# Optimization experiments

Hardware: AMD Instinct MI355X
Metric: run time of the kernel (lower is better)

The kernel has to match this reference:

```python
import jax, jax.numpy as jnp
import numpy as np

B, N, D, H = 2, 2048, 1024, 16
HD = D // H

def setup_inputs() -> dict:
    key = jax.random.key(0)
    ks = jax.random.split(key, 8)
    s = lambda fan_in: 1.0 / np.sqrt(fan_in)
    return {
        "x": jax.random.normal(ks[0], (B, N, D), jnp.float32),
        "coverage": jax.random.uniform(ks[1], (B, N, 1), jnp.float32),
        "w_qkv": jax.random.normal(ks[2], (D, 3 * D), jnp.float32) * s(D),
        "w_out": jax.random.normal(ks[3], (D, D), jnp.float32) * s(D),
        "b_out": jnp.zeros((D,), jnp.float32),
        "w_ce1": jax.random.normal(ks[4], (1, D // 4), jnp.float32),
        "b_ce1": jnp.zeros((D // 4,), jnp.float32),
        "w_ce2": jax.random.normal(ks[5], (D // 4, H), jnp.float32) * s(D // 4),
        "b_ce2": jnp.zeros((H,), jnp.float32),
        "w_fg1": jax.random.normal(ks[6], (D, D // 4), jnp.float32) * s(D),
        "b_fg1": jnp.zeros((D // 4,), jnp.float32),
        "w_fg2": jax.random.normal(ks[7], (D // 4, 1), jnp.float32) * s(D // 4),
        "b_fg2": jnp.zeros((1,), jnp.float32),
    }

def reference(x, coverage, w_qkv, w_out, b_out, w_ce1, b_ce1, w_ce2, b_ce2,
              w_fg1, b_fg1, w_fg2, b_fg2):
    b, n, d = x.shape
    h = w_ce2.shape[1]
    hd = d // h
    scale = hd ** -0.5
    qkv = x @ w_qkv  # (B,N,3D)
    q, k, v = jnp.split(qkv, 3, axis=-1)
    q = q.reshape(b, n, h, hd).transpose(0, 2, 1, 3)  # (B,H,N,hd)
    k = k.reshape(b, n, h, hd).transpose(0, 2, 1, 3)
    v = v.reshape(b, n, h, hd).transpose(0, 2, 1, 3)
    attn = jnp.einsum("bhnd,bhmd->bhnm", q, k) * scale  # (B,H,N,N)
    # coverage bias: MLP(1 -> D/4 -> H), broadcast over query dim
    cov = jax.nn.silu(coverage @ w_ce1 + b_ce1) @ w_ce2 + b_ce2  # (B,N,H)
    cov_bias = cov.transpose(0, 2, 1)[:, :, None, :]  # (B,H,1,N)
    # fusion gate on mean-pooled features
    x_pooled = x.mean(axis=1)  # (B,D)
    g = jax.nn.sigmoid(jax.nn.silu(x_pooled @ w_fg1 + b_fg1) @ w_fg2 + b_fg2)  # (B,1)
    g = g[:, :, None, None]  # (B,1,1,1)
    # g*(attn+bias) + (1-g)*attn == attn + g*bias (exact same math)
    attn = attn + g * cov_bias
    attn = jax.nn.softmax(attn, axis=-1)
    out = jnp.einsum("bhnm,bhmd->bhnd", attn, v)  # (B,H,N,hd)
    out = out.transpose(0, 2, 1, 3).reshape(b, n, d)
    return out @ w_out + b_out
```

## Files before the change

### kernel.cpp

```cpp
#include <hip/hip_runtime.h>
#include <math.h>

typedef __bf16 bf16_t;
typedef __bf16 bf16x8 __attribute__((ext_vector_type(8)));
typedef __bf16 bf16x4 __attribute__((ext_vector_type(4)));
typedef float f32x4 __attribute__((ext_vector_type(4)));

#define MFMA16(a, b, c) __builtin_amdgcn_mfma_f32_16x16x32_bf16((a), (b), (c), 0, 0, 0)

constexpr int Bc = 2, Nc = 2048, Dc = 1024, Hc = 16, HDc = 64;
constexpr float C1 = 0.18033688011112042f;
constexpr float LOG2E = 1.4426950408889634f;

__device__ __forceinline__ void glds16(const bf16_t* g, bf16_t* l) {
    __builtin_amdgcn_global_load_lds(
        (const __attribute__((address_space(1))) unsigned int*)g,
        (__attribute__((address_space(3))) unsigned int*)l, 16, 0, 0);
}

__global__ __launch_bounds__(256) void prep_all(const float* __restrict__ x,
                                                const float* __restrict__ w_qkv,
                                                const float* __restrict__ w_out,
                                                const float* __restrict__ coverage,
                                                const float* __restrict__ w_ce1,
                                                const float* __restrict__ b_ce1,
                                                const float* __restrict__ w_ce2,
                                                const float* __restrict__ b_ce2,
                                                bf16_t* __restrict__ Xb,
                                                bf16_t* __restrict__ Wt,
                                                bf16_t* __restrict__ WoT,
                                                float* __restrict__ pooled,
                                                float* __restrict__ biasbuf) {
    __shared__ bf16_t tile[64 * 66];
    int blk = blockIdx.x, t = threadIdx.x;
    if (blk < 512) {
        int row0 = blk * 8;
        int b = row0 >> 11;
        int c = t * 4;
        float s0 = 0.f, s1 = 0.f, s2 = 0.f, s3 = 0.f;
#pragma unroll
        for (int rr = 0; rr < 8; ++rr) {
            size_t off = (size_t)(row0 + rr) * 1024 + c;
            float4 v = *(const float4*)(x + off);
            bf16x4 o = { (bf16_t)v.x, (bf16_t)v.y, (bf16_t)v.z, (bf16_t)v.w };
            *(bf16x4*)(Xb + off) = o;
            s0 += v.x; s1 += v.y; s2 += v.z; s3 += v.w;
        }
        atomicAdd(&pooled[b * 1024 + c + 0], s0);
        atomicAdd(&pooled[b * 1024 + c + 1], s1);
        atomicAdd(&pooled[b * 1024 + c + 2], s2);
        atomicAdd(&pooled[b * 1024 + c + 3], s3);
    } else if (blk < 1536) {
        int idx = blk - 512;
        int cx = idx & 63, ry = idx >> 6;
        const float* src; bf16_t* dst; int C;
        if (cx < 48) { src = w_qkv; dst = Wt; C = 3072; }
        else         { src = w_out; dst = WoT; C = 1024; cx -= 48; }
        const int R = 1024;
        int r0 = ry * 64, c0 = cx * 64;
        int cl = t & 63, rl = t >> 6;
#pragma unroll
        for (int p = 0; p < 16; ++p) {
            int r = p * 4 + rl;
            tile[r * 66 + cl] = (bf16_t)src[(size_t)(r0 + r) * C + c0 + cl];
        }
        __syncthreads();
#pragma unroll
        for (int p = 0; p < 16; ++p) {
            int r = p * 4 + rl;
            dst[(size_t)(c0 + r) * R + r0 + cl] = tile[cl * 66 + r];
        }
    } else {
        int cb = blk - 1536;
        int h = t & 15;
        int gn = cb * 16 + (t >> 4);
        int b = gn >> 11, n = gn & 2047;
        float c = coverage[gn];
        float acc = b_ce2[h];
        for (int j = 0; j < 256; ++j) {
            float tv = c * w_ce1[j] + b_ce1[j];
            tv = tv / (1.0f + __expf(-tv));
            acc += tv * w_ce2[j * 16 + h];
        }
        biasbuf[((size_t)b * 16 + h) * 2048 + n] = LOG2E * acc;
    }
}

__global__ __launch_bounds__(256) void gate1(const float* __restrict__ pooled,
                                             const float* __restrict__ w_fg1,
                                             const float* __restrict__ b_fg1,
                                             const float* __restrict__ w_fg2,
                                             float* __restrict__ hacc) {
    int b = blockIdx.x >> 8, j = blockIdx.x & 255;
    int t = threadIdx.x;
    float p = 0.f;
#pragma unroll
    for (int i = 0; i < 4; ++i) {
        int d = t * 4 + i;
        p += pooled[b * 1024 + d] * w_fg1[d * 256 + j];
    }
#pragma unroll
    for (int off = 32; off > 0; off >>= 1) p += __shfl_down(p, off);
    __shared__ float red[4];
    if ((t & 63) == 0) red[t >> 6] = p;
    __syncthreads();
    if (t == 0) {
        float hj = (red[0] + red[1] + red[2] + red[3]) * (1.0f / 2048.0f) + b_fg1[j];
        hj = hj / (1.0f + __expf(-hj));
        atomicAdd(&hacc[b], hj * w_fg2[j]);
    }
}

__global__ __launch_bounds__(256) void gatebias(float* __restrict__ biasbuf,
                                                const float* __restrict__ hacc,
                                                const float* __restrict__ b_fg2) {
    int idx = (blockIdx.x * 256 + threadIdx.x) * 4;
    int b = idx >> 15;
    float g = 1.0f / (1.0f + __expf(-(hacc[b] + b_fg2[0])));
    float4 v = *(const float4*)(biasbuf + idx);
    v.x *= g; v.y *= g; v.z *= g; v.w *= g;
    *(float4*)(biasbuf + idx) = v;
}

__global__ __launch_bounds__(256) void qk_gemm(const bf16_t* __restrict__ Xb,
                                               const bf16_t* __restrict__ Wt,
                                               bf16_t* __restrict__ Q,
                                               bf16_t* __restrict__ Kb) {
    __shared__ __align__(16) bf16_t At[128 * 64];
    __shared__ __align__(16) bf16_t Bt[128 * 64];
    int t = threadIdx.x, w = t >> 6, lane = t & 63;
    int l16 = lane & 15, quad = lane >> 4;
    int wm = w & 1, wx = w >> 1;
    int m0 = blockIdx.x * 128;
    int n0 = blockIdx.y * 128;
    f32x4 acc[4][4] = {};
    int swl = l16 & 7;

    for (int k0 = 0; k0 < 1024; k0 += 64) {
#pragma unroll
        for (int i = 0; i < 4; ++i) {
            int fb = i * 4096 + w * 1024;
            int f = fb + lane * 16;
            int row = f >> 7;
            int ch = (f >> 4) & 7;
            int sc = ch ^ (row & 7);
            glds16(Wt + (size_t)(n0 + row) * 1024 + k0 + sc * 8, At + (fb >> 1));
            glds16(Xb + (size_t)(m0 + row) * 1024 + k0 + sc * 8, Bt + (fb >> 1));
        }
        __syncthreads();
#pragma unroll
        for (int s = 0; s < 2; ++s) {
            bf16x8 afr[4], bfr[4];
#pragma unroll
            for (int mi = 0; mi < 4; ++mi)
                afr[mi] = *(const bf16x8*)(At + (wm * 64 + mi * 16 + l16) * 64 + (((s * 4 + quad) ^ swl) * 8));
#pragma unroll
            for (int ni = 0; ni < 4; ++ni)
                bfr[ni] = *(const bf16x8*)(Bt + (wx * 64 + ni * 16 + l16) * 64 + (((s * 4 + quad) ^ swl) * 8));
#pragma unroll
            for (int mi = 0; mi < 4; ++mi)
#pragma unroll
                for (int ni = 0; ni < 4; ++ni)
                    acc[mi][ni] = MFMA16(afr[mi], bfr[ni], acc[mi][ni]);
        }
        __syncthreads();
    }

    int sec = n0 >> 10;
    bf16_t* dst = (sec == 0 ? Q : Kb);
#pragma unroll
    for (int mi = 0; mi < 4; ++mi) {
        int gc = n0 + wm * 64 + mi * 16 + quad * 4;
        int dcol = gc & 1023;
        int h = dcol >> 6, hd = dcol & 63;
#pragma unroll
        for (int ni = 0; ni < 4; ++ni) {
            int gx = m0 + wx * 64 + ni * 16 + l16;
            int b = gx >> 11, n = gx & 2047;
            size_t bh = (size_t)(b * 16 + h);
            bf16x4 pk = { (bf16_t)acc[mi][ni][0], (bf16_t)acc[mi][ni][1],
                          (bf16_t)acc[mi][ni][2], (bf16_t)acc[mi][ni][3] };
            *(bf16x4*)(dst + (bh * 2048 + n) * 64 + hd) = pk;
        }
    }
}

__global__ __launch_bounds__(256) void v_gemm(const bf16_t* __restrict__ Xb,
                                              const bf16_t* __restrict__ Wt,
                                              bf16_t* __restrict__ Vt) {
    __shared__ __align__(16) bf16_t At[128 * 64];
    __shared__ __align__(16) bf16_t Bt[128 * 64];
    int t = threadIdx.x, w = t >> 6, lane = t & 63;
    int l16 = lane & 15, quad = lane >> 4;
    int wm = w & 1, wx = w >> 1;
    int n0 = blockIdx.x * 128;
    int m0 = blockIdx.y * 128;
    const bf16_t* WtV = Wt + (size_t)2048 * 1024;
    f32x4 acc[4][4] = {};
    int swl = l16 & 7;

    for (int k0 = 0; k0 < 1024; k0 += 64) {
#pragma unroll
        for (int i = 0; i < 4; ++i) {
            int fb = i * 4096 + w * 1024;
            int f = fb + lane * 16;
            int row = f >> 7;
            int ch = (f >> 4) & 7;
            int sc = ch ^ (row & 7);
            glds16(Xb + (size_t)(m0 + row) * 1024 + k0 + sc * 8, At + (fb >> 1));
            glds16(WtV + (size_t)(n0 + row) * 1024 + k0 + sc * 8, Bt + (fb >> 1));
        }
        __syncthreads();
#pragma unroll
        for (int s = 0; s < 2; ++s) {
            bf16x8 afr[4], bfr[4];
#pragma unroll
            for (int mi = 0; mi < 4; ++mi)
                afr[mi] = *(const bf16x8*)(At + (wm * 64 + mi * 16 + l16) * 64 + (((s * 4 + quad) ^ swl) * 8));
#pragma unroll
            for (int ni = 0; ni < 4; ++ni)
                bfr[ni] = *(const bf16x8*)(Bt + (wx * 64 + ni * 16 + l16) * 64 + (((s * 4 + quad) ^ swl) * 8));
#pragma unroll
            for (int mi = 0; mi < 4; ++mi)
#pragma unroll
                for (int ni = 0; ni < 4; ++ni)
                    acc[mi][ni] = MFMA16(afr[mi], bfr[ni], acc[mi][ni]);
        }
        __syncthreads();
    }

#pragma unroll
    for (int mi = 0; mi < 4; ++mi) {
        int rowx = m0 + wm * 64 + mi * 16 + quad * 4;
        int b = rowx >> 11, n = rowx & 2047;
        int np = (n & ~31) + ((n >> 2) & 3) * 8 + ((n >> 4) & 1) * 4;
#pragma unroll
        for (int ni = 0; ni < 4; ++ni) {
            int colv = n0 + wx * 64 + ni * 16 + l16;
            int h = colv >> 6, hd = colv & 63;
            bf16x4 pk = { (bf16_t)acc[mi][ni][0], (bf16_t)acc[mi][ni][1],
                          (bf16_t)acc[mi][ni][2], (bf16_t)acc[mi][ni][3] };
            *(bf16x4*)(Vt + ((size_t)(b * 16 + h) * 64 + hd) * 2048 + np) = pk;
        }
    }
}

__global__ __launch_bounds__(256) void attn_k(const bf16_t* __restrict__ Q,
                                              const bf16_t* __restrict__ Kb,
                                              const bf16_t* __restrict__ Vt,
                                              const float* __restrict__ biasbuf,
                                              bf16_t* __restrict__ O) {
    __shared__ __align__(16) bf16_t kbuf[2][64 * 64];
    __shared__ __align__(16) bf16_t vbuf[2][64 * 64];
    int t = threadIdx.x, w = t >> 6, lane = t & 63;
    int l16 = lane & 15, quad = lane >> 4;
    int bh = blockIdx.y;
    int b = bh >> 4, h = bh & 15;
    int qa = blockIdx.x * 128 + w * 32;
    const bf16_t* Qh = Q + (size_t)bh * 2048 * 64;
    const bf16_t* Kh = Kb + (size_t)bh * 2048 * 64;
    const bf16_t* Vh = Vt + (size_t)bh * 64 * 2048;
    const float* bih = biasbuf + (size_t)bh * 2048;

    int fb0 = w * 2048, fb1 = fb0 + 1024;
    int f0 = fb0 + lane * 16, f1 = fb1 + lane * 16;
    int krow0 = f0 >> 7, kch0 = ((f0 >> 4) & 7) ^ (krow0 & 7);
    int krow1 = f1 >> 7, kch1 = ((f1 >> 4) & 7) ^ (krow1 & 7);

    bf16x8 qf[2][2];
#pragma unroll
    for (int g = 0; g < 2; ++g)
#pragma unroll
        for (int dh = 0; dh < 2; ++dh)
            qf[g][dh] = *(const bf16x8*)(Qh + (size_t)(qa + g * 16 + l16) * 64 + dh * 32 + quad * 8);

    f32x4 o[2][4] = {};
    f32x4 osum[2] = {};
    const f32x4 zero = { 0.f, 0.f, 0.f, 0.f };
    int swl = l16 & 7;
    bf16x8 ones;
#pragma unroll
    for (int i = 0; i < 8; ++i) ones[i] = (bf16_t)1.0f;

    {
        glds16(Kh + (size_t)krow0 * 64 + kch0 * 8, &kbuf[0][fb0 >> 1]);
        glds16(Kh + (size_t)krow1 * 64 + kch1 * 8, &kbuf[0][fb1 >> 1]);
        glds16(Vh + (size_t)krow0 * 2048 + kch0 * 8, &vbuf[0][fb0 >> 1]);
        glds16(Vh + (size_t)krow1 * 2048 + kch1 * 8, &vbuf[0][fb1 >> 1]);
    }

    for (int it = 0; it < 32; ++it) {
        int j0 = it * 64, sel = it & 1;
        __syncthreads();
        if (it + 1 < 32) {
            int jn = j0 + 64, sn = sel ^ 1;
            glds16(Kh + (size_t)(jn + krow0) * 64 + kch0 * 8, &kbuf[sn][fb0 >> 1]);
            glds16(Kh + (size_t)(jn + krow1) * 64 + kch1 * 8, &kbuf[sn][fb1 >> 1]);
            glds16(Vh + (size_t)krow0 * 2048 + jn + kch0 * 8, &vbuf[sn][fb0 >> 1]);
            glds16(Vh + (size_t)krow1 * 2048 + jn + kch1 * 8, &vbuf[sn][fb1 >> 1]);
        }
        const bf16_t* kb = kbuf[sel];
        const bf16_t* vb = vbuf[sel];

        float4 bias[4];
#pragma unroll
        for (int kt = 0; kt < 4; ++kt)
            bias[kt] = *(const float4*)(bih + j0 + kt * 16 + quad * 4);

        f32x4 s[4][2];
#pragma unroll
        for (int kt = 0; kt < 4; ++kt) {
            bf16x8 kf0 = *(const bf16x8*)(kb + (kt * 16 + l16) * 64 + ((quad ^ swl) * 8));
            bf16x8 kf1 = *(const bf16x8*)(kb + (kt * 16 + l16) * 64 + (((4 + quad) ^ swl) * 8));
#pragma unroll
            for (int g = 0; g < 2; ++g) {
                s[kt][g] = MFMA16(kf0, qf[g][0], zero);
                s[kt][g] = MFMA16(kf1, qf[g][1], s[kt][g]);
            }
        }

#pragma unroll
        for (int kt = 0; kt < 4; ++kt) {
            const float* bp = (const float*)&bias[kt];
#pragma unroll
            for (int g = 0; g < 2; ++g)
#pragma unroll
                for (int r = 0; r < 4; ++r)
                    s[kt][g][r] = __builtin_amdgcn_exp2f(s[kt][g][r] * C1 + bp[r]);
        }

        bf16x8 pf[2][2];
#pragma unroll
        for (int g = 0; g < 2; ++g)
#pragma unroll
            for (int pv = 0; pv < 2; ++pv) {
                bf16x8 tmp;
#pragma unroll
                for (int i = 0; i < 4; ++i) {
                    tmp[i]     = (bf16_t)s[2 * pv][g][i];
                    tmp[i + 4] = (bf16_t)s[2 * pv + 1][g][i];
                }
                pf[g][pv] = tmp;
            }

#pragma unroll
        for (int dt = 0; dt < 4; ++dt) {
            const bf16_t* vrow = vb + (dt * 16 + l16) * 64;
#pragma unroll
            for (int pv = 0; pv < 2; ++pv) {
                bf16x8 vf = *(const bf16x8*)(vrow + (((pv * 4 + quad) ^ swl) * 8));
#pragma unroll
                for (int g = 0; g < 2; ++g)
                    o[g][dt] = MFMA16(pf[g][pv], vf, o[g][dt]);
            }
        }
#pragma unroll
        for (int g = 0; g < 2; ++g) {
            osum[g] = MFMA16(pf[g][0], ones, osum[g]);
            osum[g] = MFMA16(pf[g][1], ones, osum[g]);
        }
    }

#pragma unroll
    for (int g = 0; g < 2; ++g) {
        float rinv[4];
#pragma unroll
        for (int r = 0; r < 4; ++r) rinv[r] = 1.0f / osum[g][r];
#pragma unroll
        for (int dt = 0; dt < 4; ++dt)
#pragma unroll
            for (int r = 0; r < 4; ++r) {
                int row = qa + g * 16 + quad * 4 + r;
                O[(size_t)(b * 2048 + row) * 1024 + h * 64 + dt * 16 + l16] =
                    (bf16_t)(o[g][dt][r] * rinv[r]);
            }
    }
}

__global__ __launch_bounds__(256) void out_gemm(const bf16_t* __restrict__ A,
                                                const bf16_t* __restrict__ Wt,
                                                const float* __restrict__ bias,
                                                float* __restrict__ Cout) {
    __shared__ __align__(16) bf16_t At[64 * 64];
    __shared__ __align__(16) bf16_t Bt[128 * 64];
    int t = threadIdx.x, w = t >> 6, lane = t & 63;
    int l16 = lane & 15, quad = lane >> 4;
    int wm = w & 1, wx = w >> 1;
    int m0 = blockIdx.x * 128;
    int n0 = blockIdx.y * 64;
    f32x4 acc[2][4] = {};
    int swl = l16 & 7;

    for (int k0 = 0; k0 < 1024; k0 += 64) {
#pragma unroll
        for (int i = 0; i < 2; ++i) {
            int fb = i * 4096 + w * 1024;
            int f = fb + lane * 16;
            int row = f >> 7;
            int ch = (f >> 4) & 7;
            int sc = ch ^ (row & 7);
            glds16(Wt + (size_t)(n0 + row) * 1024 + k0 + sc * 8, At + (fb >> 1));
        }
#pragma unroll
        for (int i = 0; i < 4; ++i) {
            int fb = i * 4096 + w * 1024;
            int f = fb + lane * 16;
            int row = f >> 7;
            int ch = (f >> 4) & 7;
            int sc = ch ^ (row & 7);
            glds16(A + (size_t)(m0 + row) * 1024 + k0 + sc * 8, Bt + (fb >> 1));
        }
        __syncthreads();
#pragma unroll
        for (int s = 0; s < 2; ++s) {
            bf16x8 afr[2], bfr[4];
#pragma unroll
            for (int mi = 0; mi < 2; ++mi)
                afr[mi] = *(const bf16x8*)(At + (wm * 32 + mi * 16 + l16) * 64 + (((s * 4 + quad) ^ swl) * 8));
#pragma unroll
            for (int ni = 0; ni < 4; ++ni)
                bfr[ni] = *(const bf16x8*)(Bt + (wx * 64 + ni * 16 + l16) * 64 + (((s * 4 + quad) ^ swl) * 8));
#pragma unroll
            for (int mi = 0; mi < 2; ++mi)
#pragma unroll
                for (int ni = 0; ni < 4; ++ni)
                    acc[mi][ni] = MFMA16(afr[mi], bfr[ni], acc[mi][ni]);
        }
        __syncthreads();
    }

#pragma unroll
    for (int mi = 0; mi < 2; ++mi) {
        int gc = n0 + wm * 32 + mi * 16 + quad * 4;
        float4 bv = *(const float4*)(bias + gc);
#pragma unroll
        for (int ni = 0; ni < 4; ++ni) {
            int gx = m0 + wx * 64 + ni * 16 + l16;
            float4 ov = { acc[mi][ni][0] + bv.x, acc[mi][ni][1] + bv.y,
                          acc[mi][ni][2] + bv.z, acc[mi][ni][3] + bv.w };
            *(float4*)(Cout + (size_t)gx * 1024 + gc) = ov;
        }
    }
}

extern "C" void kernel_launch(void* const* d_in, const int* in_sizes, int n_in,
                              void* d_out, int out_size, void* d_ws, size_t ws_size,
                              hipStream_t stream) {
    const float* x     = (const float*)d_in[0];
    const float* cov   = (const float*)d_in[1];
    const float* w_qkv = (const float*)d_in[2];
    const float* w_out = (const float*)d_in[3];
    const float* b_out = (const float*)d_in[4];
    const float* w_ce1 = (const float*)d_in[5];
    const float* b_ce1 = (const float*)d_in[6];
    const float* w_ce2 = (const float*)d_in[7];
    const float* b_ce2 = (const float*)d_in[8];
    const float* w_fg1 = (const float*)d_in[9];
    const float* b_fg1 = (const float*)d_in[10];
    const float* w_fg2 = (const float*)d_in[11];
    const float* b_fg2 = (const float*)d_in[12];

    char* ws = (char*)d_ws;
    bf16_t* Wt     = (bf16_t*)(ws);
    bf16_t* WoT    = (bf16_t*)(ws + 6291456);
    bf16_t* Xb     = (bf16_t*)(ws + 8388608);
    bf16_t* Qb     = (bf16_t*)(ws + 16777216);
    bf16_t* Kbb    = (bf16_t*)(ws + 25165824);
    bf16_t* Vt     = (bf16_t*)(ws + 33554432);
    bf16_t* Ob     = (bf16_t*)(ws + 41943040);
    float*  pooled = (float*)(ws + 50331648);
    float*  hacc   = (float*)(ws + 50339840);
    float*  biasb  = (float*)(ws + 50340096);

    hipMemsetAsync(pooled, 0, 8192 + 256, stream);
    prep_all<<<1792, 256, 0, stream>>>(x, w_qkv, w_out, cov, w_ce1, b_ce1, w_ce2, b_ce2,
                                       Xb, Wt, WoT, pooled, biasb);
    gate1<<<512, 256, 0, stream>>>(pooled, w_fg1, b_fg1, w_fg2, hacc);
    gatebias<<<64, 256, 0, stream>>>(biasb, hacc, b_fg2);
    qk_gemm<<<dim3(32, 16), 256, 0, stream>>>(Xb, Wt, Qb, Kbb);
    v_gemm<<<dim3(8, 32), 256, 0, stream>>>(Xb, Wt, Vt);
    attn_k<<<dim3(16, 32), 256, 0, stream>>>(Qb, Kbb, Vt, biasb, Ob);
    out_gemm<<<dim3(32, 16), 256, 0, stream>>>(Ob, WoT, b_out, (float*)d_out);
}
```

Before: 280.2 us.

## Split attention over two KV halves and merge QK and V projection launches

The attention kernel now splits the key/value sequence into two halves along a new grid dimension. Each half writes unnormalized partial outputs and row sums, and out_gemm adds the two halves and normalizes them while staging its A tile. The separate QK and V projection kernels are fused into one 768-block launch, and the workspace is re-laid out so the partials reuse the dead Xb/Wt space. The aim is more attention blocks for better CU occupancy and fewer launches, at the cost of extra partial-output traffic and register-staged loads in out_gemm.

After: 300.9 us. +7.4%, slower.

```diff
diff --git a/kernel.cpp b/kernel.cpp
--- a/kernel.cpp
+++ b/kernel.cpp
@@ -8,7 +8,6 @@
 
 #define MFMA16(a, b, c) __builtin_amdgcn_mfma_f32_16x16x32_bf16((a), (b), (c), 0, 0, 0)
 
-constexpr int Bc = 2, Nc = 2048, Dc = 1024, Hc = 16, HDc = 64;
 constexpr float C1 = 0.18033688011112042f;
 constexpr float LOG2E = 1.4426950408889634f;
 
@@ -122,125 +121,116 @@
     *(float4*)(biasbuf + idx) = v;
 }
 
-__global__ __launch_bounds__(256) void qk_gemm(const bf16_t* __restrict__ Xb,
-                                               const bf16_t* __restrict__ Wt,
-                                               bf16_t* __restrict__ Q,
-                                               bf16_t* __restrict__ Kb) {
+__global__ __launch_bounds__(256) void qkv_gemm(const bf16_t* __restrict__ Xb,
+                                                const bf16_t* __restrict__ Wt,
+                                                bf16_t* __restrict__ Q,
+                                                bf16_t* __restrict__ Kb,
+                                                bf16_t* __restrict__ Vt) {
     __shared__ __align__(16) bf16_t At[128 * 64];
     __shared__ __align__(16) bf16_t Bt[128 * 64];
     int t = threadIdx.x, w = t >> 6, lane = t & 63;
     int l16 = lane & 15, quad = lane >> 4;
     int wm = w & 1, wx = w >> 1;
-    int m0 = blockIdx.x * 128;
-    int n0 = blockIdx.y * 128;
+    int swl = l16 & 7;
+    int bx = blockIdx.x;
     f32x4 acc[4][4] = {};
-    int swl = l16 & 7;
-
-    for (int k0 = 0; k0 < 1024; k0 += 64) {
-#pragma unroll
-        for (int i = 0; i < 4; ++i) {
-            int fb = i * 4096 + w * 1024;
-            int f = fb + lane * 16;
-            int row = f >> 7;
-            int ch = (f >> 4) & 7;
-            int sc = ch ^ (row & 7);
-            glds16(Wt + (size_t)(n0 + row) * 1024 + k0 + sc * 8, At + (fb >> 1));
-            glds16(Xb + (size_t)(m0 + row) * 1024 + k0 + sc * 8, Bt + (fb >> 1));
-        }
-        __syncthreads();
-#pragma unroll
-        for (int s = 0; s < 2; ++s) {
-            bf16x8 afr[4], bfr[4];
-#pragma unroll
-            for (int mi = 0; mi < 4; ++mi)
-                afr[mi] = *(const bf16x8*)(At + (wm * 64 + mi * 16 + l16) * 64 + (((s * 4 + quad) ^ swl) * 8));
-#pragma unroll
-            for (int ni = 0; ni < 4; ++ni)
-                bfr[ni] = *(const bf16x8*)(Bt + (wx * 64 + ni * 16 + l16) * 64 + (((s * 4 + quad) ^ swl) * 8));
-#pragma unroll
-            for (int mi = 0; mi < 4; ++mi)
+
+    if (bx < 512) {
+        int m0 = (bx & 31) * 128;
+        int n0 = (bx >> 5) * 128;
+        for (int k0 = 0; k0 < 1024; k0 += 64) {
+#pragma unroll
+            for (int i = 0; i < 4; ++i) {
+                int fb = i * 4096 + w * 1024;
+                int f = fb + lane * 16;
+                int row = f >> 7;
+                int ch = (f >> 4) & 7;
+                int sc = ch ^ (row & 7);
+                glds16(Wt + (size_t)(n0 + row) * 1024 + k0 + sc * 8, At + (fb >> 1));
+                glds16(Xb + (size_t)(m0 + row) * 1024 + k0 + sc * 8, Bt + (fb >> 1));
+            }
+            __syncthreads();
+#pragma unroll
+            for (int s = 0; s < 2; ++s) {
+                bf16x8 afr[4], bfr[4];
+#pragma unroll
+                for (int mi = 0; mi < 4; ++mi)
+                    afr[mi] = *(const bf16x8*)(At + (wm * 64 + mi * 16 + l16) * 64 + (((s * 4 + quad) ^ swl) * 8));
 #pragma unroll
                 for (int ni = 0; ni < 4; ++ni)
-                    acc[mi][ni] = MFMA16(afr[mi], bfr[ni], acc[mi][ni]);
-        }
-        __syncthreads();
-    }
-
-    int sec = n0 >> 10;
-    bf16_t* dst = (sec == 0 ? Q : Kb);
-#pragma unroll
-    for (int mi = 0; mi < 4; ++mi) {
-        int gc = n0 + wm * 64 + mi * 16 + quad * 4;
-        int dcol = gc & 1023;
-        int h = dcol >> 6, hd = dcol & 63;
-#pragma unroll
-        for (int ni = 0; ni < 4; ++ni) {
-            int gx = m0 + wx * 64 + ni * 16 + l16;
-            int b = gx >> 11, n = gx & 2047;
-            size_t bh = (size_t)(b * 16 + h);
-            bf16x4 pk = { (bf16_t)acc[mi][ni][0], (bf16_t)acc[mi][ni][1],
-                          (bf16_t)acc[mi][ni][2], (bf16_t)acc[mi][ni][3] };
-            *(bf16x4*)(dst + (bh * 2048 + n) * 64 + hd) = pk;
-        }
-    }
-}
-
-__global__ __launch_bounds__(256) void v_gemm(const bf16_t* __restrict__ Xb,
-                                              const bf16_t* __restrict__ Wt,
-                                              bf16_t* __restrict__ Vt) {
-    __shared__ __align__(16) bf16_t At[128 * 64];
-    __shared__ __align__(16) bf16_t Bt[128 * 64];
-    int t = threadIdx.x, w = t >> 6, lane = t & 63;
-    int l16 = lane & 15, quad = lane >> 4;
-    int wm = w & 1, wx = w >> 1;
-    int n0 = blockIdx.x * 128;
-    int m0 = blockIdx.y * 128;
-    const bf16_t* WtV = Wt + (size_t)2048 * 1024;
-    f32x4 acc[4][4] = {};
-    int swl = l16 & 7;
-
-    for (int k0 = 0; k0 < 1024; k0 += 64) {
-#pragma unroll
-        for (int i = 0; i < 4; ++i) {
-            int fb = i * 4096 + w * 1024;
-            int f = fb + lane * 16;
-            int row = f >> 7;
-            int ch = (f >> 4) & 7;
-            int sc = ch ^ (row & 7);
-            glds16(Xb + (size_t)(m0 + row) * 1024 + k0 + sc * 8, At + (fb >> 1));
-            glds16(WtV + (size_t)(n0 + row) * 1024 + k0 + sc * 8, Bt + (fb >> 1));
-        }
-        __syncthreads();
-#pragma unroll
-        for (int s = 0; s < 2; ++s) {
-            bf16x8 afr[4], bfr[4];
-#pragma unroll
-            for (int mi = 0; mi < 4; ++mi)
-                afr[mi] = *(const bf16x8*)(At + (wm * 64 + mi * 16 + l16) * 64 + (((s * 4 + quad) ^ swl) * 8));
-#pragma unroll
-            for (int ni = 0; ni < 4; ++ni)
-                bfr[ni] = *(const bf16x8*)(Bt + (wx * 64 + ni * 16 + l16) * 64 + (((s * 4 + quad) ^ swl) * 8));
-#pragma unroll
-            for (int mi = 0; mi < 4; ++mi)
+                    bfr[ni] = *(const bf16x8*)(Bt + (wx * 64 + ni * 16 + l16) * 64 + (((s * 4 + quad) ^ swl) * 8));
+#pragma unroll
+                for (int mi = 0; mi < 4; ++mi)
+#pragma unroll
+                    for (int ni = 0; ni < 4; ++ni)
+                        acc[mi][ni] = MFMA16(afr[mi], bfr[ni], acc[mi][ni]);
+            }
+            __syncthreads();
+        }
+        int sec = n0 >> 10;
+        bf16_t* dst = (sec == 0 ? Q : Kb);
+#pragma unroll
+        for (int mi = 0; mi < 4; ++mi) {
+            int gc = n0 + wm * 64 + mi * 16 + quad * 4;
+            int dcol = gc & 1023;
+            int h = dcol >> 6, hd = dcol & 63;
+#pragma unroll
+            for (int ni = 0; ni < 4; ++ni) {
+                int gx = m0 + wx * 64 + ni * 16 + l16;
+                int b = gx >> 11, n = gx & 2047;
+                size_t bh = (size_t)(b * 16 + h);
+                bf16x4 pk = { (bf16_t)acc[mi][ni][0], (bf16_t)acc[mi][ni][1],
+                              (bf16_t)acc[mi][ni][2], (bf16_t)acc[mi][ni][3] };
+                *(bf16x4*)(dst + (bh * 2048 + n) * 64 + hd) = pk;
+            }
+        }
+    } else {
+        int idx = bx - 512;
+        int n0 = (idx & 7) * 128;
+        int m0 = (idx >> 3) * 128;
+        const bf16_t* WtV = Wt + (size_t)2048 * 1024;
+        for (int k0 = 0; k0 < 1024; k0 += 64) {
+#pragma unroll
+            for (int i = 0; i < 4; ++i) {
+                int fb = i * 4096 + w * 1024;
+                int f = fb + lane * 16;
+                int row = f >> 7;
+                int ch = (f >> 4) & 7;
+                int sc = ch ^ (row & 7);
+                glds16(Xb + (size_t)(m0 + row) * 1024 + k0 + sc * 8, At + (fb >> 1));
+                glds16(WtV + (size_t)(n0 + row) * 1024 + k0 + sc * 8, Bt + (fb >> 1));
+            }
+            __syncthreads();
+#pragma unroll
+            for (int s = 0; s < 2; ++s) {
+                bf16x8 afr[4], bfr[4];
+#pragma unroll
+                for (int mi = 0; mi < 4; ++mi)
+                    afr[mi] = *(const bf16x8*)(At + (wm * 64 + mi * 16 + l16) * 64 + (((s * 4 + quad) ^ swl) * 8));
 #pragma unroll
                 for (int ni = 0; ni < 4; ++ni)
-                    acc[mi][ni] = MFMA16(afr[mi], bfr[ni], acc[mi][ni]);
-        }
-        __syncthreads();
-    }
-
-#pragma unroll
-    for (int mi = 0; mi < 4; ++mi) {
-        int rowx = m0 + wm * 64 + mi * 16 + quad * 4;
-        int b = rowx >> 11, n = rowx & 2047;
-        int np = (n & ~31) + ((n >> 2) & 3) * 8 + ((n >> 4) & 1) * 4;
-#pragma unroll
-        for (int ni = 0; ni < 4; ++ni) {
-            int colv = n0 + wx * 64 + ni * 16 + l16;
-            int h = colv >> 6, hd = colv & 63;
-            bf16x4 pk = { (bf16_t)acc[mi][ni][0], (bf16_t)acc[mi][ni][1],
-                          (bf16_t)acc[mi][ni][2], (bf16_t)acc[mi][ni][3] };
-            *(bf16x4*)(Vt + ((size_t)(b * 16 + h) * 64 + hd) * 2048 + np) = pk;
+                    bfr[ni] = *(const bf16x8*)(Bt + (wx * 64 + ni * 16 + l16) * 64 + (((s * 4 + quad) ^ swl) * 8));
+#pragma unroll
+                for (int mi = 0; mi < 4; ++mi)
+#pragma unroll
+                    for (int ni = 0; ni < 4; ++ni)
+                        acc[mi][ni] = MFMA16(afr[mi], bfr[ni], acc[mi][ni]);
+            }
+            __syncthreads();
+        }
+#pragma unroll
+        for (int mi = 0; mi < 4; ++mi) {
+            int rowx = m0 + wm * 64 + mi * 16 + quad * 4;
+            int b = rowx >> 11, n = rowx & 2047;
+            int np = (n & ~31) + ((n >> 2) & 3) * 8 + ((n >> 4) & 1) * 4;
+#pragma unroll
+            for (int ni = 0; ni < 4; ++ni) {
+                int colv = n0 + wx * 64 + ni * 16 + l16;
+                int h = colv >> 6, hd = colv & 63;
+                bf16x4 pk = { (bf16_t)acc[mi][ni][0], (bf16_t)acc[mi][ni][1],
+                              (bf16_t)acc[mi][ni][2], (bf16_t)acc[mi][ni][3] };
+                *(bf16x4*)(Vt + ((size_t)(b * 16 + h) * 64 + hd) * 2048 + np) = pk;
+            }
         }
     }
 }
@@ -249,18 +239,20 @@
                                               const bf16_t* __restrict__ Kb,
                                               const bf16_t* __restrict__ Vt,
                                               const float* __restrict__ biasbuf,
-                                              bf16_t* __restrict__ O) {
+                                              bf16_t* __restrict__ opart,
+                                              float* __restrict__ spart) {
     __shared__ __align__(16) bf16_t kbuf[2][64 * 64];
     __shared__ __align__(16) bf16_t vbuf[2][64 * 64];
     int t = threadIdx.x, w = t >> 6, lane = t & 63;
     int l16 = lane & 15, quad = lane >> 4;
     int bh = blockIdx.y;
-    int b = bh >> 4, h = bh & 15;
+    int jh = blockIdx.z;
     int qa = blockIdx.x * 128 + w * 32;
     const bf16_t* Qh = Q + (size_t)bh * 2048 * 64;
     const bf16_t* Kh = Kb + (size_t)bh * 2048 * 64;
     const bf16_t* Vh = Vt + (size_t)bh * 64 * 2048;
     const float* bih = biasbuf + (size_t)bh * 2048;
+    int jbase = jh * 1024;
 
     int fb0 = w * 2048, fb1 = fb0 + 1024;
     int f0 = fb0 + lane * 16, f1 = fb1 + lane * 16;
@@ -283,16 +275,16 @@
     for (int i = 0; i < 8; ++i) ones[i] = (bf16_t)1.0f;
 
     {
-        glds16(Kh + (size_t)krow0 * 64 + kch0 * 8, &kbuf[0][fb0 >> 1]);
-        glds16(Kh + (size_t)krow1 * 64 + kch1 * 8, &kbuf[0][fb1 >> 1]);
-        glds16(Vh + (size_t)krow0 * 2048 + kch0 * 8, &vbuf[0][fb0 >> 1]);
-        glds16(Vh + (size_t)krow1 * 2048 + kch1 * 8, &vbuf[0][fb1 >> 1]);
-    }
-
-    for (int it = 0; it < 32; ++it) {
-        int j0 = it * 64, sel = it & 1;
+        glds16(Kh + (size_t)(jbase + krow0) * 64 + kch0 * 8, &kbuf[0][fb0 >> 1]);
+        glds16(Kh + (size_t)(jbase + krow1) * 64 + kch1 * 8, &kbuf[0][fb1 >> 1]);
+        glds16(Vh + (size_t)krow0 * 2048 + jbase + kch0 * 8, &vbuf[0][fb0 >> 1]);
+        glds16(Vh + (size_t)krow1 * 2048 + jbase + kch1 * 8, &vbuf[0][fb1 >> 1]);
+    }
+
+    for (int it = 0; it < 16; ++it) {
+        int j0 = jbase + it * 64, sel = it & 1;
         __syncthreads();
-        if (it + 1 < 32) {
+        if (it + 1 < 16) {
             int jn = j0 + 64, sn = sel ^ 1;
             glds16(Kh + (size_t)(jn + krow0) * 64 + kch0 * 8, &kbuf[sn][fb0 >> 1]);
             glds16(Kh + (size_t)(jn + krow1) * 64 + kch1 * 8, &kbuf[sn][fb1 >> 1]);
@@ -361,24 +353,28 @@
         }
     }
 
+    bf16_t* op = opart + ((size_t)(jh * 32 + bh) * 2048) * 64;
+    float* sp = spart + (size_t)(jh * 32 + bh) * 2048;
 #pragma unroll
     for (int g = 0; g < 2; ++g) {
-        float rinv[4];
-#pragma unroll
-        for (int r = 0; r < 4; ++r) rinv[r] = 1.0f / osum[g][r];
 #pragma unroll
         for (int dt = 0; dt < 4; ++dt)
 #pragma unroll
             for (int r = 0; r < 4; ++r) {
                 int row = qa + g * 16 + quad * 4 + r;
-                O[(size_t)(b * 2048 + row) * 1024 + h * 64 + dt * 16 + l16] =
-                    (bf16_t)(o[g][dt][r] * rinv[r]);
-            }
-    }
-}
-
-__global__ __launch_bounds__(256) void out_gemm(const bf16_t* __restrict__ A,
-                                                const bf16_t* __restrict__ Wt,
+                op[(size_t)row * 64 + dt * 16 + l16] = (bf16_t)o[g][dt][r];
+            }
+        if (l16 == 0) {
+#pragma unroll
+            for (int r = 0; r < 4; ++r)
+                sp[qa + g * 16 + quad * 4 + r] = osum[g][r];
+        }
+    }
+}
+
+__global__ __launch_bounds__(256) void out_gemm(const bf16_t* __restrict__ opart,
+                                                const float* __restrict__ spart,
+                                                const bf16_t* __restrict__ WoT,
                                                 const float* __restrict__ bias,
                                                 float* __restrict__ Cout) {
     __shared__ __align__(16) bf16_t At[64 * 64];
@@ -388,10 +384,18 @@
     int wm = w & 1, wx = w >> 1;
     int m0 = blockIdx.x * 128;
     int n0 = blockIdx.y * 64;
+    int b = m0 >> 11;
+    int m0l = m0 & 2047;
     f32x4 acc[2][4] = {};
     int swl = l16 & 7;
 
     for (int k0 = 0; k0 < 1024; k0 += 64) {
+        int h = k0 >> 6;
+        size_t bh = (size_t)(b * 16 + h);
+        const bf16_t* o0 = opart + (bh * 2048 + m0l) * 64;
+        const bf16_t* o1 = opart + ((bh + 32) * 2048 + m0l) * 64;
+        const float* s0p = spart + bh * 2048 + m0l;
+        const float* s1p = spart + (bh + 32) * 2048 + m0l;
 #pragma unroll
         for (int i = 0; i < 2; ++i) {
             int fb = i * 4096 + w * 1024;
@@ -399,16 +403,22 @@
             int row = f >> 7;
             int ch = (f >> 4) & 7;
             int sc = ch ^ (row & 7);
-            glds16(Wt + (size_t)(n0 + row) * 1024 + k0 + sc * 8, At + (fb >> 1));
-        }
-#pragma unroll
-        for (int i = 0; i < 4; ++i) {
-            int fb = i * 4096 + w * 1024;
-            int f = fb + lane * 16;
+            glds16(WoT + (size_t)(n0 + row) * 1024 + k0 + sc * 8, At + (fb >> 1));
+        }
+#pragma unroll
+        for (int pass = 0; pass < 4; ++pass) {
+            int f = (pass * 256 + t) * 16;
             int row = f >> 7;
             int ch = (f >> 4) & 7;
             int sc = ch ^ (row & 7);
-            glds16(A + (size_t)(m0 + row) * 1024 + k0 + sc * 8, Bt + (fb >> 1));
+            bf16x8 oa = *(const bf16x8*)(o0 + (size_t)row * 64 + sc * 8);
+            bf16x8 ob = *(const bf16x8*)(o1 + (size_t)row * 64 + sc * 8);
+            float rinv = __builtin_amdgcn_rcpf(s0p[row] + s1p[row]);
+            bf16x8 wv;
+#pragma unroll
+            for (int i = 0; i < 8; ++i)
+                wv[i] = (bf16_t)(((float)oa[i] + (float)ob[i]) * rinv);
+            *(bf16x8*)(Bt + (f >> 1)) = wv;
         }
         __syncthreads();
 #pragma unroll
@@ -461,24 +471,24 @@
     const float* b_fg2 = (const float*)d_in[12];
 
     char* ws = (char*)d_ws;
-    bf16_t* Wt     = (bf16_t*)(ws);
-    bf16_t* WoT    = (bf16_t*)(ws + 6291456);
-    bf16_t* Xb     = (bf16_t*)(ws + 8388608);
+    bf16_t* opart  = (bf16_t*)(ws);
+    bf16_t* Xb     = (bf16_t*)(ws);
+    bf16_t* Wt     = (bf16_t*)(ws + 8388608);
     bf16_t* Qb     = (bf16_t*)(ws + 16777216);
     bf16_t* Kbb    = (bf16_t*)(ws + 25165824);
     bf16_t* Vt     = (bf16_t*)(ws + 33554432);
-    bf16_t* Ob     = (bf16_t*)(ws + 41943040);
-    float*  pooled = (float*)(ws + 50331648);
-    float*  hacc   = (float*)(ws + 50339840);
-    float*  biasb  = (float*)(ws + 50340096);
+    bf16_t* WoT    = (bf16_t*)(ws + 41943040);
+    float*  biasb  = (float*)(ws + 44040192);
+    float*  spart  = (float*)(ws + 44564480);
+    float*  pooled = (float*)(ws + 45088768);
+    float*  hacc   = (float*)(ws + 45096960);
 
     hipMemsetAsync(pooled, 0, 8192 + 256, stream);
     prep_all<<<1792, 256, 0, stream>>>(x, w_qkv, w_out, cov, w_ce1, b_ce1, w_ce2, b_ce2,
                                        Xb, Wt, WoT, pooled, biasb);
     gate1<<<512, 256, 0, stream>>>(pooled, w_fg1, b_fg1, w_fg2, hacc);
     gatebias<<<64, 256, 0, stream>>>(biasb, hacc, b_fg2);
-    qk_gemm<<<dim3(32, 16), 256, 0, stream>>>(Xb, Wt, Qb, Kbb);
-    v_gemm<<<dim3(8, 32), 256, 0, stream>>>(Xb, Wt, Vt);
-    attn_k<<<dim3(16, 32), 256, 0, stream>>>(Qb, Kbb, Vt, biasb, Ob);
-    out_gemm<<<dim3(32, 16), 256, 0, stream>>>(Ob, WoT, b_out, (float*)d_out);
-}
+    qkv_gemm<<<768, 256, 0, stream>>>(Xb, Wt, Qb, Kbb, Vt);
+    attn_k<<<dim3(16, 32, 2), 256, 0, stream>>>(Qb, Kbb, Vt, biasb, opart, spart);
+    out_gemm<<<dim3(32, 16), 256, 0, stream>>>(opart, spart, WoT, b_out, (float*)d_out);
+}
```
